# Kernel optimization log

Measured on AMD Instinct MI355X. Metric: run time of the kernel, lower is better.

Reference implementation:

```python
import jax, jax.numpy as jnp
import numpy as np


def setup_inputs() -> dict:
    key = jax.random.key(0)
    ks = jax.random.split(key, 8)
    B, De, Do, T, H, W = 4, 128, 512, 4, 30, 52
    s = 0.05  # weight init scale
    return {
        "m_in": jax.random.normal(ks[0], (B, De, T, H, W), jnp.float32),
        "m_out": jax.random.normal(ks[1], (B, Do, T, H, W), jnp.float32),
        "q_in": jax.random.normal(ks[2], (B, De, H, W), jnp.float32),
        "q_out": jax.random.normal(ks[3], (B, Do, H, W), jnp.float32),
        "wr": jax.random.normal(ks[4], (Do, 2 * Do), jnp.float32) * s,
        "br": jnp.zeros((Do,), jnp.float32),
        "wu": jax.random.normal(ks[5], (Do, 2 * Do), jnp.float32) * s,
        "bu": jnp.zeros((Do,), jnp.float32),
        "wc": jax.random.normal(ks[6], (Do, 2 * Do), jnp.float32) * s,
        "bc": jnp.zeros((Do,), jnp.float32),
    }


def reference(m_in, m_out, q_in, q_out, wr, br, wu, bu, wc, bc):
    B, De, T, H, W = m_in.shape
    Do = m_out.shape[1]
    PROP_LAYERS = 5

    # --- memory read: pairwise frame attention (bmm + softmax + bmm) ---
    # keys: all T memory frames flattened; queries: current frame.
    mi = m_in.reshape(B, De, T * H * W)            # [B, De, THW]
    qi = q_in.reshape(B, De, H * W)                # [B, De, HW]
    p = jnp.einsum('bdk,bdq->bkq', mi, qi) / (De ** 0.5)  # [B, THW, HW]
    p = jax.nn.softmax(p, axis=1)                  # softmax over memory locations (dim=1 in torch)
    mem = jnp.einsum('bok,bkq->boq', m_out.reshape(B, Do, T * H * W), p)
    mem = mem.reshape(B, Do, H, W)                 # mem_mean; identical every propagate layer

    # --- ConvGRU_h (kernel_size=1 => per-pixel linear gates) ---
    def conv1x1(w, b, x):
        return jnp.einsum('oc,bchw->bohw', w, x) + b[None, :, None, None]

    def gru(x, h):
        xh = jnp.concatenate([x, h], axis=1)                       # [B, 2*Do, H, W]
        r = jax.nn.sigmoid(conv1x1(wr, br, xh))
        u = jax.nn.sigmoid(conv1x1(wu, bu, xh))
        c = jnp.tanh(conv1x1(wc, bc, jnp.concatenate([x, r * h], axis=1)))
        return h * (1.0 - u) + u * c

    q0 = q_out
    q = q_out
    for _ in range(PROP_LAYERS):
        q = gru(q, mem)  # original: q_out = ConvGRU_h(q_out, mem_mean)
    return jnp.concatenate([q, q0], axis=1)  # [B, 2*Do, H, W]
```

## Files before the change

### kernel.cpp

```cpp
#include <hip/hip_runtime.h>
#include <hip/hip_bf16.h>
#include <math.h>

typedef unsigned short u16;
typedef __attribute__((ext_vector_type(8))) short bf16x8;
typedef __attribute__((ext_vector_type(4))) float f32x4;

__device__ __forceinline__ u16 f2bf(float f) {
  union { float f; unsigned u; } x; x.f = f;
  unsigned r = x.u + 0x7fffu + ((x.u >> 16) & 1u);
  return (u16)(r >> 16);
}
__device__ __forceinline__ float bf2f(u16 h) {
  union { unsigned u; float f; } x; x.u = ((unsigned)h) << 16;
  return x.f;
}
__device__ __forceinline__ float sigmf(float x) {
  x = fminf(fmaxf(x, -30.f), 30.f);
  return 1.f / (1.f + __expf(-x));
}
__device__ __forceinline__ float tanh_fast(float x) {
  x = fminf(fmaxf(x, -15.f), 15.f);
  float t = __expf(2.f * x);
  return (t - 1.f) / (t + 1.f);
}

template<int N> __device__ __forceinline__ void wait_vmcnt() {
  if constexpr (N == 0)       asm volatile("s_waitcnt vmcnt(0)" ::: "memory");
  else if constexpr (N == 4)  asm volatile("s_waitcnt vmcnt(4)" ::: "memory");
  else if constexpr (N == 6)  asm volatile("s_waitcnt vmcnt(6)" ::: "memory");
  else if constexpr (N == 8)  asm volatile("s_waitcnt vmcnt(8)" ::: "memory");
  else if constexpr (N == 9)  asm volatile("s_waitcnt vmcnt(9)" ::: "memory");
  else if constexpr (N == 10) asm volatile("s_waitcnt vmcnt(10)" ::: "memory");
  else static_assert(N == 0, "add vmcnt case");
}

#define NB 4
#define DE 128
#define DO_ 512
#define HW 1560
#define THW 6240
#define NP 1664
#define KP 6272
#define PROP 5
#define PVSPLIT 7
#define PVKC 896

template<int MODE, int BMT, int BKT>
__device__ __forceinline__
void gemm_core(const u16* __restrict__ A, const u16* __restrict__ Bt,
               int K, int lda, int ldb, long a_bs, long b_bs,
               void* __restrict__ out0v, long o0_bs, int ld0,
               u16* __restrict__ out1, long o1_bs, int ld1,
               u16* __restrict__ out2, long o2_bs,
               const void* __restrict__ e0v, long e0_bs,
               const void* __restrict__ e1v, long e1_bs,
               const void* __restrict__ e2v, long e2_bs,
               const void* __restrict__ e3v, long e3_bs,
               int nvalid, float scale)
{
  constexpr int WR = BMT / 64;
  constexpr int WC = 4 / WR;
  constexpr int NF = 8 / WC;
  constexpr int KK = BKT / 32;
  constexpr int ASLOT = BMT * BKT / 8;
  constexpr int BSLOT = 128 * BKT / 8;
  constexpr int NISS = (ASLOT + BSLOT) / 256;
  constexpr int RSH = (BMT == 128) ? 7 : 6;
  __shared__ u16 lds[2][ASLOT + BSLOT][8];

  const int tid = threadIdx.x;
  const int wave = tid >> 6, lane = tid & 63;
  const int kg = lane >> 4, lr = lane & 15;
  const int wrw = wave / WC, wcw = wave % WC;
  const long b = blockIdx.z;
  const int m0 = blockIdx.x * BMT, n0 = blockIdx.y * 128;
  A += b * a_bs; Bt += b * b_bs;

  float* out0f = (float*)out0v;
  u16* out0h = (u16*)out0v;
  const float* e0f = (const float*)e0v;
  const u16* e0h = (const u16*)e0v;
  const u16* e1h = (const u16*)e1v;
  const u16* e2h = (const u16*)e2v;
  const u16* e3h = (const u16*)e3v;

  auto stage = [&](int buf, int kt) {
#pragma unroll
    for (int i = 0; i < NISS; ++i) {
      int s = tid + 256 * i;
      const u16* src;
      if (s < ASLOT) {
        int row = s & (BMT - 1), g = s >> RSH;
        src = A + (long)(m0 + row) * lda + kt + g * 8;
      } else {
        int s2 = s - ASLOT;
        int row = s2 & 127, g = s2 >> 7;
        src = Bt + (long)(n0 + row) * ldb + kt + g * 8;
      }
      __builtin_amdgcn_global_load_lds(
          (const __attribute__((address_space(1))) void*)src,
          (__attribute__((address_space(3))) void*)&lds[buf][wave * 64 + 256 * i][0],
          16, 0, 0);
    }
  };

  f32x4 acc[4][NF];
#pragma unroll
  for (int m = 0; m < 4; ++m)
#pragma unroll
    for (int n = 0; n < NF; ++n) acc[m][n] = (f32x4){0.f, 0.f, 0.f, 0.f};

  const int nt = K / BKT;
  stage(0, 0);
  for (int t = 0; t < nt; ++t) {
    int cur = t & 1;
    if (t + 1 < nt) {
      stage(cur ^ 1, (t + 1) * BKT);
      wait_vmcnt<NISS>();
    } else {
      wait_vmcnt<0>();
    }
    __builtin_amdgcn_s_barrier();
    bf16x8 af[KK][4], bfr[KK][NF];
#pragma unroll
    for (int kk = 0; kk < KK; ++kk) {
#pragma unroll
      for (int m = 0; m < 4; ++m)
        af[kk][m] = *(const bf16x8*)&lds[cur][(kk * 4 + kg) * BMT + wrw * 64 + m * 16 + lr][0];
#pragma unroll
      for (int n = 0; n < NF; ++n)
        bfr[kk][n] = *(const bf16x8*)&lds[cur][ASLOT + (kk * 4 + kg) * 128 + (wcw * NF + n) * 16 + lr][0];
    }
#pragma unroll
    for (int kk = 0; kk < KK; ++kk)
#pragma unroll
      for (int m = 0; m < 4; ++m)
#pragma unroll
        for (int n = 0; n < NF; ++n)
          acc[m][n] = __builtin_amdgcn_mfma_f32_16x16x32_bf16(af[kk][m], bfr[kk][n], acc[m][n], 0, 0, 0);
    __builtin_amdgcn_s_barrier();
  }

  if constexpr (MODE == 0) {
    float rs[4][4];
#pragma unroll
    for (int m = 0; m < 4; ++m)
#pragma unroll
      for (int j = 0; j < 4; ++j) rs[m][j] = 0.f;
#pragma unroll
    for (int m = 0; m < 4; ++m) {
      int rloc = wrw * 64 + m * 16 + kg * 4;
#pragma unroll
      for (int n = 0; n < NF; ++n) {
        int col = n0 + (wcw * NF + n) * 16 + lr;
#pragma unroll
        for (int j = 0; j < 4; ++j) {
          long row = m0 + rloc + j;
          float p = __expf(acc[m][n][j] * scale);
          bool valid = (col < nvalid);
          out1[b * o1_bs + row * ld1 + col] = valid ? f2bf(p) : (u16)0;
          rs[m][j] += valid ? p : 0.f;
        }
      }
    }
#pragma unroll
    for (int m = 0; m < 4; ++m)
#pragma unroll
      for (int j = 0; j < 4; ++j) {
#pragma unroll
        for (int msk = 1; msk < 16; msk <<= 1)
          rs[m][j] += __shfl_xor(rs[m][j], msk, 64);
      }
    float* zbuf = (float*)lds;
    if (lr == 0) {
#pragma unroll
      for (int m = 0; m < 4; ++m)
#pragma unroll
        for (int j = 0; j < 4; ++j)
          zbuf[wcw * 128 + wrw * 64 + m * 16 + kg * 4 + j] = rs[m][j];
    }
    __syncthreads();
    if (tid < 128)
      out0f[b * o0_bs + (long)blockIdx.y * NP + (m0 + tid)] = zbuf[tid] + zbuf[128 + tid];
    return;
  }

#pragma unroll
  for (int m = 0; m < 4; ++m) {
    int rloc = wrw * 64 + m * 16 + kg * 4;
#pragma unroll
    for (int n = 0; n < NF; ++n) {
      int col = n0 + (wcw * NF + n) * 16 + lr;
#pragma unroll
      for (int j = 0; j < 4; ++j) {
        long row = m0 + rloc + j;
        float v = acc[m][n][j];
        if constexpr (MODE == 2) {
          out1[b * o1_bs + row * ld1 + col] = f2bf(v + e0f[col]);
        } else if constexpr (MODE == 3) {
          if (col < 1024) {
            float gt = sigmf(v + bf2f(e0h[b * e0_bs + row * 1024 + col]));
            if (col < 512)
              out1[b * o1_bs + row * ld1 + 512 + col] =
                  f2bf(gt * bf2f(e1h[b * e1_bs + row * 512 + col]));
            else
              out0h[b * o0_bs + row * ld0 + (col - 512)] = f2bf(gt);
          } else {
            out2[b * o2_bs + row * 512 + (col - 1024)] = f2bf(v);
          }
        } else if constexpr (MODE == 4) {
          float cg = tanh_fast(v + bf2f(e3h[b * e3_bs + row * 512 + col]) + e0f[col]);
          float u = bf2f(e1h[b * e1_bs + row * 512 + col]);
          float mm = bf2f(e2h[b * e2_bs + row * 512 + col]);
          float x = mm * (1.f - u) + u * cg;
          out1[b * o1_bs + row * ld1 + col] = f2bf(x);
          if (out0f && row < nvalid)
            out0f[b * o0_bs + (long)col * ld0 + row] = x;
        }
      }
    }
  }
}

#define GEMM_ARGS                                                              \
  const u16* __restrict__ A, const u16* __restrict__ Bt, int K, int lda,       \
  int ldb, long a_bs, long b_bs, void* __restrict__ out0v, long o0_bs,         \
  int ld0, u16* __restrict__ out1, long o1_bs, int ld1,                        \
  u16* __restrict__ out2, long o2_bs,                                          \
  const void* __restrict__ e0v, long e0_bs, const void* __restrict__ e1v,      \
  long e1_bs, const void* __restrict__ e2v, long e2_bs,                        \
  const void* __restrict__ e3v, long e3_bs, int nvalid, float scale
#define GEMM_PASS A, Bt, K, lda, ldb, a_bs, b_bs, out0v, o0_bs, ld0, out1,     \
  o1_bs, ld1, out2, o2_bs, e0v, e0_bs, e1v, e1_bs, e2v, e2_bs, e3v, e3_bs,     \
  nvalid, scale

__global__ __launch_bounds__(256) void gk_scores(GEMM_ARGS) { gemm_core<0, 128, 32>(GEMM_PASS); }
__global__ __launch_bounds__(256) void gk_chru(GEMM_ARGS)   { gemm_core<2, 64, 64>(GEMM_PASS); }
__global__ __launch_bounds__(256) void gk_gates(GEMM_ARGS)  { gemm_core<3, 128, 64>(GEMM_PASS); }
__global__ __launch_bounds__(256) void gk_cand(GEMM_ARGS)   { gemm_core<4, 64, 64>(GEMM_PASS); }

__global__ __launch_bounds__(256, 2)
void gemm_pv(const u16* __restrict__ Pt, const u16* __restrict__ moutb,
             u16* __restrict__ Ppart)
{
  const int bid = blockIdx.x;
  const int xcd = bid & 7, i = bid >> 3;
  const int s = xcd * 91 + i;
  const int pair = s / 26, mb = s - pair * 26;
  const int b = pair / PVSPLIT, z = pair - b * PVSPLIT;
  const int m0 = mb * 64;
  const int k0 = z * PVKC;

  const u16* A = Pt + (long)b * NP * KP;
  const u16* B0;
  {
    const u16* Bb = moutb + (long)b * DO_ * KP;
    B0 = Bb + (long)((threadIdx.x >> 6) * 128 + (threadIdx.x & 15)) * KP +
         ((threadIdx.x & 63) >> 4) * 8;
  }

  __shared__ u16 lds[3][2048];
  const int tid = threadIdx.x;
  const int wave = tid >> 6, lane = tid & 63;
  const int kg = lane >> 4, lr = lane & 15;

  auto stage = [&](int buf, int kt) {
    int row = tid & 63;
    const u16* src = A + (long)(m0 + row) * KP + kt + (tid >> 6) * 8;
    __builtin_amdgcn_global_load_lds(
        (const __attribute__((address_space(1))) void*)src,
        (__attribute__((address_space(3))) void*)&lds[buf][(wave * 64) * 8],
        16, 0, 0);
  };

  f32x4 acc[4][8];
#pragma unroll
  for (int m = 0; m < 4; ++m)
#pragma unroll
    for (int n = 0; n < 8; ++n) acc[m][n] = (f32x4){0.f, 0.f, 0.f, 0.f};

  bf16x8 bra[8], brb[8];
  stage(0, k0);
#pragma unroll
  for (int n = 0; n < 8; ++n)
    bra[n] = *(const bf16x8*)&B0[(long)n * 16 * KP + k0];
  stage(1, k0 + 32);

#define PV_STEP(T, BUF, SBUF, BU, BL, DOB, DOS, VM)                              \
  {                                                                              \
    if (DOB) {                                                                   \
      _Pragma("unroll") for (int n = 0; n < 8; ++n)                              \
          BL[n] = *(const bf16x8*)&B0[(long)n * 16 * KP + k0 + ((T) + 1) * 32];  \
    }                                                                            \
    if (DOS) stage(SBUF, k0 + ((T) + 2) * 32);                                   \
    wait_vmcnt<VM>();                                                            \
    __builtin_amdgcn_s_barrier();                                                \
    bf16x8 af[4];                                                                \
    _Pragma("unroll") for (int m = 0; m < 4; ++m)                                \
        af[m] = *(const bf16x8*)&lds[BUF][(kg * 64 + m * 16 + lr) * 8];          \
    _Pragma("unroll") for (int m = 0; m < 4; ++m)                                \
        _Pragma("unroll") for (int n = 0; n < 8; ++n)                            \
            acc[m][n] = __builtin_amdgcn_mfma_f32_16x16x32_bf16(af[m], BU[n],    \
                                                                acc[m][n], 0, 0, 0); \
    __builtin_amdgcn_s_barrier();                                                \
  }

  for (int tt = 0; tt < 4; ++tt) {
    PV_STEP(6 * tt + 0, 0, 2, bra, brb, 1, 1, 10);
    PV_STEP(6 * tt + 1, 1, 0, brb, bra, 1, 1, 10);
    PV_STEP(6 * tt + 2, 2, 1, bra, brb, 1, 1, 10);
    PV_STEP(6 * tt + 3, 0, 2, brb, bra, 1, 1, 10);
    PV_STEP(6 * tt + 4, 1, 0, bra, brb, 1, 1, 10);
    PV_STEP(6 * tt + 5, 2, 1, brb, bra, 1, 1, 10);
  }
  PV_STEP(24, 0, 2, bra, brb, 1, 1, 10);
  PV_STEP(25, 1, 0, brb, bra, 1, 1, 10);
  PV_STEP(26, 2, 1, bra, brb, 1, 0, 9);
  PV_STEP(27, 0, 2, brb, bra, 0, 0, 0);
#undef PV_STEP

  u16* out = Ppart + (long)(b * PVSPLIT + z) * NP * DO_;
#pragma unroll
  for (int m = 0; m < 4; ++m) {
#pragma unroll
    for (int n = 0; n < 8; ++n) {
      int col = wave * 128 + n * 16 + lr;
#pragma unroll
      for (int j = 0; j < 4; ++j) {
        int row = m0 + m * 16 + kg * 4 + j;
        out[(long)row * DO_ + col] = f2bf(acc[m][n][j]);
      }
    }
  }
}

__global__ void k_transpose_cast(const float* __restrict__ in, u16* __restrict__ out,
                                 int R, int C, int Cp, int out_ld,
                                 long in_bs, long out_bs) {
  __shared__ float t[32][33];
  long b = blockIdx.z;
  int c0 = blockIdx.x * 32, r0 = blockIdx.y * 32;
  int tx = threadIdx.x, ty = threadIdx.y;
#pragma unroll
  for (int i = 0; i < 32; i += 8) {
    int r = r0 + ty + i, c = c0 + tx;
    t[ty + i][tx] = (r < R && c < C) ? in[b * in_bs + (long)r * C + c] : 0.f;
  }
  __syncthreads();
#pragma unroll
  for (int i = 0; i < 32; i += 8) {
    int c = c0 + ty + i, r = r0 + tx;
    if (c < Cp && r < R)
      out[b * out_bs + (long)c * out_ld + r] = f2bf(t[tx][ty + i]);
  }
}

__global__ void k_cast_pad4(const float* __restrict__ in, u16* __restrict__ out,
                            int Cin, int Cout, long in_bs, long out_bs) {
  int c4 = (blockIdx.x * 256 + threadIdx.x) * 4;
  int r = blockIdx.y;
  long b = blockIdx.z;
  if (c4 >= Cout) return;
  uint2 o = {0u, 0u};
  if (c4 < Cin) {
    float4 v = *(const float4*)&in[b * in_bs + (long)r * Cin + c4];
    o.x = (unsigned)f2bf(v.x) | ((unsigned)f2bf(v.y) << 16);
    o.y = (unsigned)f2bf(v.z) | ((unsigned)f2bf(v.w) << 16);
  }
  *(uint2*)&out[b * out_bs + (long)r * Cout + c4] = o;
}

__global__ void k_build_w(const float* __restrict__ wr_, const float* __restrict__ wu_,
                          const float* __restrict__ wc_,
                          u16* __restrict__ wruh, u16* __restrict__ wruxc,
                          u16* __restrict__ wch) {
  int k = blockIdx.x * 256 + threadIdx.x;
  int m = blockIdx.y;
  if (k >= 512) return;
  if (m < 1024) {
    const float* src = (m < 512) ? wr_ : wu_;
    wruh[m * 512 + k] = f2bf(src[(m & 511) * 1024 + 512 + k]);
  } else if (m < 2560) {
    int n = m - 1024;
    const float* src = (n < 512) ? wr_ : ((n < 1024) ? wu_ : wc_);
    wruxc[n * 512 + k] = f2bf(src[(n & 511) * 1024 + k]);
  } else {
    int n = m - 2560;
    wch[n * 512 + k] = f2bf(wc_[n * 1024 + 512 + k]);
  }
}

__global__ void k_bias_ru(const float* __restrict__ br_, const float* __restrict__ bu_,
                          float* __restrict__ bias) {
  int i = blockIdx.x * 256 + threadIdx.x;
  if (i < 1024) bias[i] = (i < 512) ? br_[i] : bu_[i - 512];
}

__global__ void k_invz(const float* __restrict__ Zp, float* __restrict__ invZ) {
  int t = blockIdx.x * 256 + threadIdx.x;
  if (t >= NB * NP) return;
  int b = t / NP, q = t - b * NP;
  const float* base = Zp + (long)b * 49 * NP + q;
  float s = 0.f;
#pragma unroll
  for (int nb = 0; nb < 49; ++nb) s += base[(long)nb * NP];
  invZ[t] = 1.f / s;
}

__global__ void k_reduce_mem(const u16* __restrict__ Ppart, const float* __restrict__ invZ,
                             u16* __restrict__ memTb) {
  long t = (long)blockIdx.x * 256 + threadIdx.x;
  const long bs = (long)NP * DO_;
  if (t >= (long)NB * bs / 8) return;
  long flat = t * 8;
  int b = (int)(flat / bs);
  long r = flat - (long)b * bs;
  int q = (int)(r / DO_);
  float s[8];
#pragma unroll
  for (int e = 0; e < 8; ++e) s[e] = 0.f;
#pragma unroll
  for (int z = 0; z < PVSPLIT; ++z) {
    uint4 v = *(const uint4*)&Ppart[(long)(b * PVSPLIT + z) * bs + r];
    s[0] += bf2f((u16)(v.x & 0xffff)); s[1] += bf2f((u16)(v.x >> 16));
    s[2] += bf2f((u16)(v.y & 0xffff)); s[3] += bf2f((u16)(v.y >> 16));
    s[4] += bf2f((u16)(v.z & 0xffff)); s[5] += bf2f((u16)(v.z >> 16));
    s[6] += bf2f((u16)(v.w & 0xffff)); s[7] += bf2f((u16)(v.w >> 16));
  }
  float iz = invZ[b * NP + q];
  uint4 o;
  o.x = (unsigned)f2bf(s[0] * iz) | ((unsigned)f2bf(s[1] * iz) << 16);
  o.y = (unsigned)f2bf(s[2] * iz) | ((unsigned)f2bf(s[3] * iz) << 16);
  o.z = (unsigned)f2bf(s[4] * iz) | ((unsigned)f2bf(s[5] * iz) << 16);
  o.w = (unsigned)f2bf(s[6] * iz) | ((unsigned)f2bf(s[7] * iz) << 16);
  *(uint4*)&memTb[(long)b * bs + r] = o;
}

__global__ void k_copy_q0(const float4* __restrict__ src, float4* __restrict__ dst) {
  int idx = blockIdx.x * 256 + threadIdx.x;
  long b = blockIdx.z;
  const long n4 = (long)DO_ * HW / 4;
  if (idx < n4)
    dst[b * ((long)1024 * HW / 4) + n4 + idx] = src[b * n4 + idx];
}

extern "C" void kernel_launch(void* const* d_in, const int* in_sizes, int n_in,
                              void* d_out, int out_size, void* d_ws, size_t ws_size,
                              hipStream_t stream) {
  const float* m_in  = (const float*)d_in[0];
  const float* m_out = (const float*)d_in[1];
  const float* q_in  = (const float*)d_in[2];
  const float* q_out = (const float*)d_in[3];
  const float* wr    = (const float*)d_in[4];
  const float* br    = (const float*)d_in[5];
  const float* wu    = (const float*)d_in[6];
  const float* bu    = (const float*)d_in[7];
  const float* wc    = (const float*)d_in[8];
  const float* bc    = (const float*)d_in[9];
  float* dout = (float*)d_out;

  char* p = (char*)d_ws;
  size_t off = 0;
  auto alloc = [&](size_t bytes) { void* r = p + off; off += (bytes + 255) & ~(size_t)255; return r; };
  u16*   miT    = (u16*)alloc((size_t)NB * KP * DE * 2);
  u16*   qiT    = (u16*)alloc((size_t)NB * NP * DE * 2);
  u16*   Pt     = (u16*)alloc((size_t)NB * NP * KP * 2);
  float* invZ   = (float*)alloc((size_t)NB * NP * 4);
  u16*   moutb  = (u16*)alloc((size_t)NB * DO_ * KP * 2);
  u16*   memTb  = (u16*)alloc((size_t)NB * NP * DO_ * 2);
  u16*   chru   = (u16*)alloc((size_t)NB * NP * 1024 * 2);
  u16*   U      = (u16*)alloc((size_t)NB * NP * DO_ * 2);
  u16*   XRb    = (u16*)alloc((size_t)NB * NP * 1024 * 2);
  float* Qfin   = (float*)alloc((size_t)NB * NP * DO_ * 4);
  (void)Qfin;
  u16*   XRa    = (u16*)alloc((size_t)NB * NP * 1024 * 2);
  u16*   Cx     = (u16*)alloc((size_t)NB * NP * 512 * 2);
  u16*   wruh   = (u16*)alloc((size_t)1024 * 512 * 2);
  u16*   wruxc  = (u16*)alloc((size_t)1536 * 512 * 2);
  u16*   wch    = (u16*)alloc((size_t)512 * 512 * 2);
  float* biasru = (float*)alloc((size_t)1024 * 4);
  u16*   Ppart  = (u16*)chru;
  float* Zp     = (float*)memTb;
  if (off > ws_size) return;

  k_build_w<<<dim3(2, 3072), 256, 0, stream>>>(wr, wu, wc, wruh, wruxc, wch);
  k_bias_ru<<<dim3(4), 256, 0, stream>>>(br, bu, biasru);
  k_cast_pad4<<<dim3(7, 512, NB), 256, 0, stream>>>(
      m_out, moutb, THW, KP, (long)DO_ * THW, (long)DO_ * KP);
  k_transpose_cast<<<dim3(196, 4, NB), dim3(32, 8), 0, stream>>>(
      m_in, miT, DE, THW, KP, DE, (long)DE * THW, (long)KP * DE);
  k_transpose_cast<<<dim3(52, 4, NB), dim3(32, 8), 0, stream>>>(
      q_in, qiT, DE, HW, NP, DE, (long)DE * HW, (long)NP * DE);
  k_transpose_cast<<<dim3(52, 16, NB), dim3(32, 8), 0, stream>>>(
      q_out, XRa, DO_, HW, NP, 1024, (long)DO_ * HW, (long)NP * 1024);

  gk_scores<<<dim3(13, 49, NB), 256, 0, stream>>>(
      qiT, miT, DE, DE, DE, (long)NP * DE, (long)KP * DE,
      Zp, (long)49 * NP, 0, Pt, (long)NP * KP, KP, nullptr, 0,
      nullptr, 0, nullptr, 0, nullptr, 0, nullptr, 0, THW, 0.08838834764831845f);
  k_invz<<<dim3(26), 256, 0, stream>>>(Zp, invZ);

  gemm_pv<<<dim3(728), 256, 0, stream>>>(Pt, moutb, Ppart);
  k_reduce_mem<<<dim3(1664), 256, 0, stream>>>(Ppart, invZ, memTb);

  gk_chru<<<dim3(26, 8, NB), 256, 0, stream>>>(
      memTb, wruh, DO_, DO_, DO_, (long)NP * DO_, 0,
      nullptr, 0, 0, chru, (long)NP * 1024, 1024, nullptr, 0,
      biasru, 0, nullptr, 0, nullptr, 0, nullptr, 0, 0, 0.f);

  u16* xr[2] = {XRa, XRb};
  for (int l = 0; l < PROP; ++l) {
    u16* cur = xr[l & 1];
    u16* nxt = xr[(l + 1) & 1];
    gk_gates<<<dim3(13, 12, NB), 256, 0, stream>>>(
        cur, wruxc, DO_, 1024, DO_, (long)NP * 1024, 0,
        U, (long)NP * DO_, DO_, cur, (long)NP * 1024, 1024,
        Cx, (long)NP * 512,
        chru, (long)NP * 1024, memTb, (long)NP * DO_, nullptr, 0,
        nullptr, 0, 0, 0.f);
    gk_cand<<<dim3(26, 4, NB), 256, 0, stream>>>(
        cur + 512, wch, DO_, 1024, DO_, (long)NP * 1024, 0,
        (l == PROP - 1) ? (void*)dout : nullptr, (long)1024 * HW, HW,
        nxt, (long)NP * 1024, 1024, nullptr, 0,
        bc, 0, U, (long)NP * DO_, memTb, (long)NP * DO_,
        Cx, (long)NP * 512, HW, 0.f);
  }

  k_copy_q0<<<dim3(780, 1, NB), 256, 0, stream>>>((const float4*)q_out, (float4*)dout);
}
```

Baseline: 655.1 us.

## Fuse score GEMM, exp and PV GEMM into one flash-attention style kernel

Replaces the separate score kernel (which wrote a full bf16 probability matrix to global memory), the inverse-normalizer kernel and the PV GEMM with one fused kernel. It computes QK^T tiles in LDS, exponentiates them, accumulates partial row sums and multiplies by m_out on the fly. Normalizer partials are summed in the reduce kernel. This removes a large global write/read of the NP×KP probability matrix, but it recomputes per-tile score MFMAs and adds extra barriers and LDS round-trips for P inside the PV loop. Like the old code, it uses an unshifted exp without a max subtraction.

```diff
diff --git a/kernel.cpp b/kernel.cpp
--- a/kernel.cpp
+++ b/kernel.cpp
@@ -30,8 +30,6 @@
   else if constexpr (N == 4)  asm volatile("s_waitcnt vmcnt(4)" ::: "memory");
   else if constexpr (N == 6)  asm volatile("s_waitcnt vmcnt(6)" ::: "memory");
   else if constexpr (N == 8)  asm volatile("s_waitcnt vmcnt(8)" ::: "memory");
-  else if constexpr (N == 9)  asm volatile("s_waitcnt vmcnt(9)" ::: "memory");
-  else if constexpr (N == 10) asm volatile("s_waitcnt vmcnt(10)" ::: "memory");
   else static_assert(N == 0, "add vmcnt case");
 }
 
@@ -45,6 +43,7 @@
 #define PROP 5
 #define PVSPLIT 7
 #define PVKC 896
+#define SCALE 0.08838834764831845f
 
 template<int MODE, int BMT, int BKT>
 __device__ __forceinline__
@@ -140,50 +139,6 @@
         for (int n = 0; n < NF; ++n)
           acc[m][n] = __builtin_amdgcn_mfma_f32_16x16x32_bf16(af[kk][m], bfr[kk][n], acc[m][n], 0, 0, 0);
     __builtin_amdgcn_s_barrier();
-  }
-
-  if constexpr (MODE == 0) {
-    float rs[4][4];
-#pragma unroll
-    for (int m = 0; m < 4; ++m)
-#pragma unroll
-      for (int j = 0; j < 4; ++j) rs[m][j] = 0.f;
-#pragma unroll
-    for (int m = 0; m < 4; ++m) {
-      int rloc = wrw * 64 + m * 16 + kg * 4;
-#pragma unroll
-      for (int n = 0; n < NF; ++n) {
-        int col = n0 + (wcw * NF + n) * 16 + lr;
-#pragma unroll
-        for (int j = 0; j < 4; ++j) {
-          long row = m0 + rloc + j;
-          float p = __expf(acc[m][n][j] * scale);
-          bool valid = (col < nvalid);
-          out1[b * o1_bs + row * ld1 + col] = valid ? f2bf(p) : (u16)0;
-          rs[m][j] += valid ? p : 0.f;
-        }
-      }
-    }
-#pragma unroll
-    for (int m = 0; m < 4; ++m)
-#pragma unroll
-      for (int j = 0; j < 4; ++j) {
-#pragma unroll
-        for (int msk = 1; msk < 16; msk <<= 1)
-          rs[m][j] += __shfl_xor(rs[m][j], msk, 64);
-      }
-    float* zbuf = (float*)lds;
-    if (lr == 0) {
-#pragma unroll
-      for (int m = 0; m < 4; ++m)
-#pragma unroll
-        for (int j = 0; j < 4; ++j)
-          zbuf[wcw * 128 + wrw * 64 + m * 16 + kg * 4 + j] = rs[m][j];
-    }
-    __syncthreads();
-    if (tid < 128)
-      out0f[b * o0_bs + (long)blockIdx.y * NP + (m0 + tid)] = zbuf[tid] + zbuf[128 + tid];
-    return;
   }
 
 #pragma unroll
@@ -235,14 +190,14 @@
   o1_bs, ld1, out2, o2_bs, e0v, e0_bs, e1v, e1_bs, e2v, e2_bs, e3v, e3_bs,     \
   nvalid, scale
 
-__global__ __launch_bounds__(256) void gk_scores(GEMM_ARGS) { gemm_core<0, 128, 32>(GEMM_PASS); }
 __global__ __launch_bounds__(256) void gk_chru(GEMM_ARGS)   { gemm_core<2, 64, 64>(GEMM_PASS); }
 __global__ __launch_bounds__(256) void gk_gates(GEMM_ARGS)  { gemm_core<3, 128, 64>(GEMM_PASS); }
 __global__ __launch_bounds__(256) void gk_cand(GEMM_ARGS)   { gemm_core<4, 64, 64>(GEMM_PASS); }
 
 __global__ __launch_bounds__(256, 2)
-void gemm_pv(const u16* __restrict__ Pt, const u16* __restrict__ moutb,
-             u16* __restrict__ Ppart)
+void gemm_fa(const u16* __restrict__ qiT, const u16* __restrict__ miT,
+             const u16* __restrict__ moutb,
+             u16* __restrict__ Ppart, float* __restrict__ Zp)
 {
   const int bid = blockIdx.x;
   const int xcd = bid & 7, i = bid >> 3;
@@ -252,73 +207,112 @@
   const int m0 = mb * 64;
   const int k0 = z * PVKC;
 
-  const u16* A = Pt + (long)b * NP * KP;
-  const u16* B0;
-  {
-    const u16* Bb = moutb + (long)b * DO_ * KP;
-    B0 = Bb + (long)((threadIdx.x >> 6) * 128 + (threadIdx.x & 15)) * KP +
-         ((threadIdx.x & 63) >> 4) * 8;
-  }
-
-  __shared__ u16 lds[3][2048];
   const int tid = threadIdx.x;
   const int wave = tid >> 6, lane = tid & 63;
   const int kg = lane >> 4, lr = lane & 15;
 
-  auto stage = [&](int buf, int kt) {
-    int row = tid & 63;
-    const u16* src = A + (long)(m0 + row) * KP + kt + (tid >> 6) * 8;
+  __shared__ u16 ldsQ[1024 * 8];
+  __shared__ u16 ldsK[2][512 * 8];
+  __shared__ u16 ldsP[64 * 40];
+
+  const u16* Qb = qiT + (long)b * NP * DE;
+  const u16* Mb = miT + (long)b * KP * DE;
+  const u16* B0 = moutb + (long)b * DO_ * KP +
+                  (long)(wave * 128 + lr) * KP + kg * 8;
+
+  auto stageK = [&](int buf, int ts) {
+#pragma unroll
+    for (int i2 = 0; i2 < 2; ++i2) {
+      int s2 = tid + 256 * i2;
+      int row = s2 & 31, g = s2 >> 5;
+      const u16* src = Mb + (long)(k0 + ts * 32 + row) * DE + g * 8;
+      __builtin_amdgcn_global_load_lds(
+          (const __attribute__((address_space(1))) void*)src,
+          (__attribute__((address_space(3))) void*)&ldsK[buf][(wave * 64 + 256 * i2) * 8],
+          16, 0, 0);
+    }
+  };
+
+#pragma unroll
+  for (int i2 = 0; i2 < 4; ++i2) {
+    int s2 = tid + 256 * i2;
+    int row = s2 & 63, g = s2 >> 6;
+    const u16* src = Qb + (long)(m0 + row) * DE + g * 8;
     __builtin_amdgcn_global_load_lds(
         (const __attribute__((address_space(1))) void*)src,
-        (__attribute__((address_space(3))) void*)&lds[buf][(wave * 64) * 8],
+        (__attribute__((address_space(3))) void*)&ldsQ[(wave * 64 + 256 * i2) * 8],
         16, 0, 0);
-  };
+  }
+  stageK(0, 0);
+  __syncthreads();
 
   f32x4 acc[4][8];
 #pragma unroll
   for (int m = 0; m < 4; ++m)
 #pragma unroll
     for (int n = 0; n < 8; ++n) acc[m][n] = (f32x4){0.f, 0.f, 0.f, 0.f};
-
-  bf16x8 bra[8], brb[8];
-  stage(0, k0);
-#pragma unroll
-  for (int n = 0; n < 8; ++n)
-    bra[n] = *(const bf16x8*)&B0[(long)n * 16 * KP + k0];
-  stage(1, k0 + 32);
-
-#define PV_STEP(T, BUF, SBUF, BU, BL, DOB, DOS, VM)                              \
+  float zacc[4] = {0.f, 0.f, 0.f, 0.f};
+  bf16x8 b_[8];
+
+#define FA_STEP(T, CUR, DOS)                                                     \
   {                                                                              \
-    if (DOB) {                                                                   \
-      _Pragma("unroll") for (int n = 0; n < 8; ++n)                              \
-          BL[n] = *(const bf16x8*)&B0[(long)n * 16 * KP + k0 + ((T) + 1) * 32];  \
+    _Pragma("unroll") for (int n = 0; n < 8; ++n)                                \
+        b_[n] = *(const bf16x8*)&B0[(long)n * 16 * KP + k0 + (T) * 32];          \
+    if (DOS) stageK((CUR) ^ 1, (T) + 1);                                         \
+    bf16x8 qf[4], kc[2][4];                                                      \
+    _Pragma("unroll") for (int kk = 0; kk < 4; ++kk)                             \
+        qf[kk] = *(const bf16x8*)&ldsQ[((kk * 4 + kg) * 64 + wave * 16 + lr) * 8]; \
+    _Pragma("unroll") for (int n = 0; n < 2; ++n)                                \
+        _Pragma("unroll") for (int kk = 0; kk < 4; ++kk)                         \
+            kc[n][kk] = *(const bf16x8*)&ldsK[CUR][((kk * 4 + kg) * 32 + n * 16 + lr) * 8]; \
+    f32x4 sacc[2];                                                               \
+    sacc[0] = (f32x4){0.f, 0.f, 0.f, 0.f};                                       \
+    sacc[1] = (f32x4){0.f, 0.f, 0.f, 0.f};                                       \
+    _Pragma("unroll") for (int kk = 0; kk < 4; ++kk)                             \
+        _Pragma("unroll") for (int n = 0; n < 2; ++n)                            \
+            sacc[n] = __builtin_amdgcn_mfma_f32_16x16x32_bf16(qf[kk], kc[n][kk], \
+                                                              sacc[n], 0, 0, 0); \
+    _Pragma("unroll") for (int n = 0; n < 2; ++n) {                              \
+      bool valid = (k0 + (T) * 32 + n * 16 + lr) < THW;                          \
+      _Pragma("unroll") for (int j = 0; j < 4; ++j) {                            \
+        float pf = valid ? __expf(sacc[n][j] * SCALE) : 0.f;                     \
+        zacc[j] += pf;                                                           \
+        ldsP[(wave * 16 + kg * 4 + j) * 40 + n * 16 + lr] = f2bf(pf);            \
+      }                                                                          \
     }                                                                            \
-    if (DOS) stage(SBUF, k0 + ((T) + 2) * 32);                                   \
-    wait_vmcnt<VM>();                                                            \
+    if (DOS) asm volatile("s_waitcnt vmcnt(2) lgkmcnt(0)" ::: "memory");         \
+    else     asm volatile("s_waitcnt vmcnt(0) lgkmcnt(0)" ::: "memory");         \
     __builtin_amdgcn_s_barrier();                                                \
-    bf16x8 af[4];                                                                \
+    bf16x8 pa[4];                                                                \
     _Pragma("unroll") for (int m = 0; m < 4; ++m)                                \
-        af[m] = *(const bf16x8*)&lds[BUF][(kg * 64 + m * 16 + lr) * 8];          \
+        pa[m] = *(const bf16x8*)&ldsP[(m * 16 + lr) * 40 + kg * 8];              \
     _Pragma("unroll") for (int m = 0; m < 4; ++m)                                \
         _Pragma("unroll") for (int n = 0; n < 8; ++n)                            \
-            acc[m][n] = __builtin_amdgcn_mfma_f32_16x16x32_bf16(af[m], BU[n],    \
+            acc[m][n] = __builtin_amdgcn_mfma_f32_16x16x32_bf16(pa[m], b_[n],    \
                                                                 acc[m][n], 0, 0, 0); \
+    asm volatile("s_waitcnt vmcnt(0) lgkmcnt(0)" ::: "memory");                  \
     __builtin_amdgcn_s_barrier();                                                \
   }
 
-  for (int tt = 0; tt < 4; ++tt) {
-    PV_STEP(6 * tt + 0, 0, 2, bra, brb, 1, 1, 10);
-    PV_STEP(6 * tt + 1, 1, 0, brb, bra, 1, 1, 10);
-    PV_STEP(6 * tt + 2, 2, 1, bra, brb, 1, 1, 10);
-    PV_STEP(6 * tt + 3, 0, 2, brb, bra, 1, 1, 10);
-    PV_STEP(6 * tt + 4, 1, 0, bra, brb, 1, 1, 10);
-    PV_STEP(6 * tt + 5, 2, 1, brb, bra, 1, 1, 10);
-  }
-  PV_STEP(24, 0, 2, bra, brb, 1, 1, 10);
-  PV_STEP(25, 1, 0, brb, bra, 1, 1, 10);
-  PV_STEP(26, 2, 1, bra, brb, 1, 0, 9);
-  PV_STEP(27, 0, 2, brb, bra, 0, 0, 0);
-#undef PV_STEP
+  for (int tp = 0; tp < 13; ++tp) {
+    FA_STEP(2 * tp, 0, 1);
+    FA_STEP(2 * tp + 1, 1, 1);
+  }
+  FA_STEP(26, 0, 1);
+  FA_STEP(27, 1, 0);
+#undef FA_STEP
+
+#pragma unroll
+  for (int j = 0; j < 4; ++j) {
+#pragma unroll
+    for (int msk = 1; msk < 16; msk <<= 1)
+      zacc[j] += __shfl_xor(zacc[j], msk, 64);
+  }
+  if (lr == 0) {
+#pragma unroll
+    for (int j = 0; j < 4; ++j)
+      Zp[((long)b * PVSPLIT + z) * NP + m0 + wave * 16 + kg * 4 + j] = zacc[j];
+  }
 
   u16* out = Ppart + (long)(b * PVSPLIT + z) * NP * DO_;
 #pragma unroll
@@ -397,18 +391,7 @@
   if (i < 1024) bias[i] = (i < 512) ? br_[i] : bu_[i - 512];
 }
 
-__global__ void k_invz(const float* __restrict__ Zp, float* __restrict__ invZ) {
-  int t = blockIdx.x * 256 + threadIdx.x;
-  if (t >= NB * NP) return;
-  int b = t / NP, q = t - b * NP;
-  const float* base = Zp + (long)b * 49 * NP + q;
-  float s = 0.f;
-#pragma unroll
-  for (int nb = 0; nb < 49; ++nb) s += base[(long)nb * NP];
-  invZ[t] = 1.f / s;
-}
-
-__global__ void k_reduce_mem(const u16* __restrict__ Ppart, const float* __restrict__ invZ,
+__global__ void k_reduce_mem(const u16* __restrict__ Ppart, const float* __restrict__ Zp,
                              u16* __restrict__ memTb) {
   long t = (long)blockIdx.x * 256 + threadIdx.x;
   const long bs = (long)NP * DO_;
@@ -420,6 +403,7 @@
   float s[8];
 #pragma unroll
   for (int e = 0; e < 8; ++e) s[e] = 0.f;
+  float zs = 0.f;
 #pragma unroll
   for (int z = 0; z < PVSPLIT; ++z) {
     uint4 v = *(const uint4*)&Ppart[(long)(b * PVSPLIT + z) * bs + r];
@@ -427,8 +411,9 @@
     s[2] += bf2f((u16)(v.y & 0xffff)); s[3] += bf2f((u16)(v.y >> 16));
     s[4] += bf2f((u16)(v.z & 0xffff)); s[5] += bf2f((u16)(v.z >> 16));
     s[6] += bf2f((u16)(v.w & 0xffff)); s[7] += bf2f((u16)(v.w >> 16));
-  }
-  float iz = invZ[b * NP + q];
+    zs += Zp[((long)b * PVSPLIT + z) * NP + q];
+  }
+  float iz = 1.f / zs;
   uint4 o;
   o.x = (unsigned)f2bf(s[0] * iz) | ((unsigned)f2bf(s[1] * iz) << 16);
   o.y = (unsigned)f2bf(s[2] * iz) | ((unsigned)f2bf(s[3] * iz) << 16);
@@ -465,8 +450,7 @@
   auto alloc = [&](size_t bytes) { void* r = p + off; off += (bytes + 255) & ~(size_t)255; return r; };
   u16*   miT    = (u16*)alloc((size_t)NB * KP * DE * 2);
   u16*   qiT    = (u16*)alloc((size_t)NB * NP * DE * 2);
-  u16*   Pt     = (u16*)alloc((size_t)NB * NP * KP * 2);
-  float* invZ   = (float*)alloc((size_t)NB * NP * 4);
+  float* Zp     = (float*)alloc((size_t)NB * PVSPLIT * NP * 4);
   u16*   moutb  = (u16*)alloc((size_t)NB * DO_ * KP * 2);
   u16*   memTb  = (u16*)alloc((size_t)NB * NP * DO_ * 2);
   u16*   chru   = (u16*)alloc((size_t)NB * NP * 1024 * 2);
@@ -481,7 +465,6 @@
   u16*   wch    = (u16*)alloc((size_t)512 * 512 * 2);
   float* biasru = (float*)alloc((size_t)1024 * 4);
   u16*   Ppart  = (u16*)chru;
-  float* Zp     = (float*)memTb;
   if (off > ws_size) return;
 
   k_build_w<<<dim3(2, 3072), 256, 0, stream>>>(wr, wu, wc, wruh, wruxc, wch);
@@ -495,14 +478,8 @@
   k_transpose_cast<<<dim3(52, 16, NB), dim3(32, 8), 0, stream>>>(
       q_out, XRa, DO_, HW, NP, 1024, (long)DO_ * HW, (long)NP * 1024);
 
-  gk_scores<<<dim3(13, 49, NB), 256, 0, stream>>>(
-      qiT, miT, DE, DE, DE, (long)NP * DE, (long)KP * DE,
-      Zp, (long)49 * NP, 0, Pt, (long)NP * KP, KP, nullptr, 0,
-      nullptr, 0, nullptr, 0, nullptr, 0, nullptr, 0, THW, 0.08838834764831845f);
-  k_invz<<<dim3(26), 256, 0, stream>>>(Zp, invZ);
-
-  gemm_pv<<<dim3(728), 256, 0, stream>>>(Pt, moutb, Ppart);
-  k_reduce_mem<<<dim3(1664), 256, 0, stream>>>(Ppart, invZ, memTb);
+  gemm_fa<<<dim3(728), 256, 0, stream>>>(qiT, miT, moutb, Ppart, Zp);
+  k_reduce_mem<<<dim3(1664), 256, 0, stream>>>(Ppart, Zp, memTb);
 
   gk_chru<<<dim3(26, 8, NB), 256, 0, stream>>>(
       memTb, wruh, DO_, DO_, DO_, (long)NP * DO_, 0,
```

After: 627.7 us. -4.2%, faster.
